# Kernel tuning notes

Hardware: AMD Instinct MI355X
Metric: run time of the kernel (lower is better)

Reference implementation:

```python
import jax, jax.numpy as jnp
import numpy as np

IN_SIZE, R = 80, 5
D = 256  # hidden size used throughout
OUT = IN_SIZE * R  # 400


def gru_cell(x, h, Wih, Whh, bih, bhh):
    # torch.nn.GRUCell semantics
    gi = x @ Wih.T + bih
    gh = h @ Whh.T + bhh
    ir, iz, in_ = jnp.split(gi, 3, axis=-1)
    hr, hz, hn = jnp.split(gh, 3, axis=-1)
    r = jax.nn.sigmoid(ir + hr)
    z = jax.nn.sigmoid(iz + hz)
    n = jnp.tanh(in_ + r * hn)
    return (1.0 - z) * n + z * h


def setup_inputs() -> dict:
    key = jax.random.key(0)
    ks = jax.random.split(key, 32)
    s = 0.05
    inp = {
        'encoder_outputs': jax.random.normal(ks[0], (128, 512, D), jnp.float32),
        'inputs': jax.random.normal(ks[1], (128, 1000, IN_SIZE), jnp.float32),
        # Prenet: Linear(400,256), Linear(256,128)
        'W1': jax.random.normal(ks[2], (256, OUT)) * s, 'b1': jnp.zeros((256,)),
        'W2': jax.random.normal(ks[3], (128, 256)) * s, 'b2': jnp.zeros((128,)),
        # attn GRUCell(384 -> 256)
        'Wih_a': jax.random.normal(ks[4], (3 * D, 128 + D)) * s,
        'Whh_a': jax.random.normal(ks[5], (3 * D, D)) * s,
        'bih_a': jnp.zeros((3 * D,)), 'bhh_a': jnp.zeros((3 * D,)),
        # Bahdanau attention: query_layer (no bias) and v: Linear(256,1,no bias)
        'Wq': jax.random.normal(ks[6], (D, D)) * s,
        'v': jax.random.normal(ks[7], (D,)) * s,
        # memory_layer Linear(256,256,no bias)
        'Wm': jax.random.normal(ks[8], (D, D)) * s,
        # pre_rnn_dec_proj Linear(512,256)
        'Wp': jax.random.normal(ks[9], (D, 2 * D)) * s, 'bp': jnp.zeros((D,)),
        # two decoder GRUCells(256 -> 256)
        'Wih_d1': jax.random.normal(ks[10], (3 * D, D)) * s,
        'Whh_d1': jax.random.normal(ks[11], (3 * D, D)) * s,
        'bih_d1': jnp.zeros((3 * D,)), 'bhh_d1': jnp.zeros((3 * D,)),
        'Wih_d2': jax.random.normal(ks[12], (3 * D, D)) * s,
        'Whh_d2': jax.random.normal(ks[13], (3 * D, D)) * s,
        'bih_d2': jnp.zeros((3 * D,)), 'bhh_d2': jnp.zeros((3 * D,)),
        # mel projection Linear(256, 400)
        'Wmel': jax.random.normal(ks[14], (OUT, D)) * s, 'bmel': jnp.zeros((OUT,)),
    }
    return inp


def reference(encoder_outputs, inputs, W1, b1, W2, b2,
              Wih_a, Whh_a, bih_a, bhh_a, Wq, v, Wm, Wp, bp,
              Wih_d1, Whh_d1, bih_d1, bhh_d1,
              Wih_d2, Whh_d2, bih_d2, bhh_d2, Wmel, bmel):
    B = encoder_outputs.shape[0]
    processed_mem = encoder_outputs @ Wm.T               # (B, T_enc, D)
    # teacher forcing: (B, T_mel, in_size) -> (T_dec, B, in_size*r)
    x = inputs.reshape(B, inputs.shape[1] // R, -1).transpose(1, 0, 2)
    # decoder input at step t is frame t-1 (zeros at t=0)
    x_shift = jnp.concatenate([jnp.zeros_like(x[:1]), x[:-1]], axis=0)

    def step(carry, x_t):
        attn_h, h1, h2, ctx = carry
        # prenet (dropout disabled: eval-mode reference)
        pre = jax.nn.relu(x_t @ W1.T + b1)
        pre = jax.nn.relu(pre @ W2.T + b2)                # (B, 128)
        cell_in = jnp.concatenate([pre, ctx], axis=-1)    # (B, 384)
        attn_h = gru_cell(cell_in, attn_h, Wih_a, Whh_a, bih_a, bhh_a)
        q = attn_h @ Wq.T                                 # (B, D)
        logits = jnp.tanh(q[:, None, :] + processed_mem) @ v  # (B, T_enc)
        align = jax.nn.softmax(logits, axis=-1)
        ctx = jnp.einsum('bt,btd->bd', align, encoder_outputs)
        dec_in = jnp.concatenate([attn_h, ctx], axis=-1) @ Wp.T + bp
        h1 = gru_cell(dec_in, h1, Wih_d1, Whh_d1, bih_d1, bhh_d1)
        dec_in = h1 + dec_in
        h2 = gru_cell(dec_in, h2, Wih_d2, Whh_d2, bih_d2, bhh_d2)
        dec_in = h2 + dec_in
        out = dec_in @ Wmel.T + bmel                      # (B, 400)
        return (attn_h, h1, h2, ctx), (out, align)

    z = jnp.zeros((B, D), encoder_outputs.dtype)
    init = (z, z, z, z)
    _, (outs, aligns) = jax.lax.scan(step, init, x_shift)
    outputs = outs.transpose(1, 0, 2)       # (B, T_dec, 400)
    alignments = aligns.transpose(1, 0, 2)  # (B, T_dec, T_enc)
    return outputs, alignments
```

## Files before the change

kernel.cpp:

```cpp
#include <hip/hip_runtime.h>

typedef _Float16 h2f __attribute__((ext_vector_type(2)));

#define LOG2E 1.44269504088896f

__device__ __forceinline__ float fexp2(float x){ return __builtin_amdgcn_exp2f(x); }
__device__ __forceinline__ float frcp (float x){ return __builtin_amdgcn_rcpf(x); }
__device__ __forceinline__ float sigm (float x){ return frcp(1.f + fexp2(-LOG2E*x)); }
__device__ __forceinline__ float tanhf2(float x){
  x = fminf(15.f, fmaxf(-15.f, x));
  float e = fexp2(2.f*LOG2E*x);
  return (e-1.f)*frcp(e+1.f);
}
__device__ __forceinline__ unsigned pkh2(float a, float b){
  h2f h; h.x = (_Float16)a; h.y = (_Float16)b;
  return __builtin_bit_cast(unsigned, h);
}

#if __has_builtin(__builtin_amdgcn_fdot2)
__device__ __forceinline__ float dot2(unsigned a, unsigned b, float c){
  return __builtin_amdgcn_fdot2(__builtin_bit_cast(h2f,a), __builtin_bit_cast(h2f,b), c, false);
}
#else
__device__ __forceinline__ float dot2(unsigned a, unsigned b, float c){
  h2f ha=__builtin_bit_cast(h2f,a), hb=__builtin_bit_cast(h2f,b);
  return c + (float)ha.x*(float)hb.x + (float)ha.y*(float)hb.y;
}
#endif

__device__ __forceinline__ void dot8_2(uint4 w, uint4 x, float& a0, float& a1){
  a0 = dot2(w.x, x.x, a0); a1 = dot2(w.y, x.y, a1);
  a0 = dot2(w.z, x.z, a0); a1 = dot2(w.w, x.w, a1);
}

template<int N, int K8>
__device__ __forceinline__ float mv(const uint4* __restrict__ W, const uint4* __restrict__ xs, int n){
  float a0 = 0.f, a1 = 0.f;
  #pragma unroll 4
  for (int k8 = 0; k8 < K8; ++k8)
    dot8_2(W[k8*N + n], xs[k8], a0, a1);
  return a0 + a1;
}

template<int N, int K8, int C>
__device__ __forceinline__ float mvc(const uint4* __restrict__ W, const uint4* __restrict__ xs, int n){
  float a0 = 0.f, a1 = 0.f;
  int k8 = 0;
  #pragma unroll 1
  for (; k8 + C <= K8; k8 += C){
    uint4 w[C];
    #pragma unroll
    for (int i = 0; i < C; ++i) w[i] = W[(size_t)(k8+i)*N + n];
    #pragma unroll
    for (int i = 0; i < C; ++i) dot8_2(w[i], xs[k8+i], a0, a1);
  }
  if constexpr (K8 % C){
    constexpr int R = K8 % C;
    uint4 w[R];
    #pragma unroll
    for (int i = 0; i < R; ++i) w[i] = W[(size_t)(k8+i)*N + n];
    #pragma unroll
    for (int i = 0; i < R; ++i) dot8_2(w[i], xs[k8+i], a0, a1);
  }
  return a0 + a1;
}

static constexpr size_t OFF_W1   = 0;
static constexpr size_t OFF_W2   = 204800;
static constexpr size_t OFF_WIHA = 270336;
static constexpr size_t OFF_WHHA = 860160;
static constexpr size_t OFF_WQ   = 1253376;
static constexpr size_t OFF_WP   = 1384448;
static constexpr size_t OFF_WD1I = 1646592;
static constexpr size_t OFF_WD1H = 2039808;
static constexpr size_t OFF_WD2I = 2433024;
static constexpr size_t OFF_WD2H = 2826240;
static constexpr size_t OFF_WMEL = 3219456;
static constexpr size_t OFF_WM   = 3424256;
static constexpr size_t OFF_TPM  = 3555328;
static constexpr size_t OFF_ENCH = 37109760;

__global__ void pack_w(const float* __restrict__ src, uint4* __restrict__ dst, int N, int K8){
  int idx = blockIdx.x*blockDim.x + threadIdx.x;
  if (idx >= N*K8) return;
  int n = idx % N, k8 = idx / N;
  const float* s = src + (size_t)n*(K8*8) + k8*8;
  dst[idx] = make_uint4(pkh2(s[0],s[1]), pkh2(s[2],s[3]), pkh2(s[4],s[5]), pkh2(s[6],s[7]));
}

__global__ void conv_enc(const float* __restrict__ enc, unsigned* __restrict__ encH){
  size_t i = blockIdx.x*(size_t)blockDim.x + threadIdx.x;
  if (i >= (size_t)128*512*128) return;
  const float2 f = *(const float2*)(enc + 2*i);
  encH[i] = pkh2(f.x, f.y);
}

__global__ __launch_bounds__(1024) void pm_kernel(const float* __restrict__ enc,
    const uint4* __restrict__ Wmp, unsigned* __restrict__ tpm)
{
  int b = blockIdx.y, tc = blockIdx.x;
  int tid = threadIdx.x;
  __shared__ __align__(16) unsigned s_e[4][128];
  if (tid < 512){
    int r = tid >> 7, d2 = tid & 127;
    const float2 f = *(const float2*)(enc + ((size_t)b*512 + tc*4 + r)*256 + 2*d2);
    s_e[r][d2] = pkh2(f.x, f.y);
  }
  __syncthreads();
  int d = tid & 255, r = tid >> 8;
  float acc = mv<256,32>(Wmp, (const uint4*)s_e[r], d);
  float tq = tanhf2(acc);
  float hi = __shfl_down(tq, 1);
  if ((d & 1) == 0)
    tpm[(size_t)b*65536 + (size_t)(d>>1)*512 + (tc*4 + r)] = pkh2(tq, hi);
}

__global__ __launch_bounds__(256) void prenet_kernel(
    const float* __restrict__ inputs,
    const float* __restrict__ b1, const float* __restrict__ b2,
    const uint4* __restrict__ W1p, const uint4* __restrict__ W2p,
    float* __restrict__ out)
{
  int t = blockIdx.x, b = blockIdx.y;
  int tid = threadIdx.x;
  __shared__ __align__(16) unsigned s_x[200];
  __shared__ __align__(16) unsigned s_p1[128];
  __shared__ float s_a[256];
  if (tid < 200){
    unsigned xv = 0u;
    if (t > 0){
      const float2 f = *(const float2*)(inputs + (size_t)b*80000 + (size_t)(t-1)*400 + 2*tid);
      xv = pkh2(f.x, f.y);
    }
    s_x[tid] = xv;
  }
  __syncthreads();
  float a = fmaxf(mv<256,50>(W1p, (const uint4*)s_x, tid) + b1[tid], 0.f);
  s_a[tid] = a;
  __syncthreads();
  if (tid < 128) s_p1[tid] = pkh2(s_a[2*tid], s_a[2*tid+1]);
  __syncthreads();
  if (tid < 128){
    float p = fmaxf(mv<128,32>(W2p, (const uint4*)s_p1, tid) + b2[tid], 0.f);
    float pN = __shfl_down(p, 1);
    if (!(tid & 1)){
      unsigned* dst = (unsigned*)(out + (size_t)10240000 + ((size_t)b*200 + t)*512);
      dst[tid>>1] = pkh2(p, pN);
    }
  }
}

__global__ __launch_bounds__(512) void mel_kernel(
    const float* __restrict__ bmel, const uint4* __restrict__ Wmelp,
    float* __restrict__ out)
{
  int t = blockIdx.x, b = blockIdx.y;
  int tid = threadIdx.x;
  __shared__ __align__(16) unsigned s_d[128];
  float* po = out + ((size_t)b*200 + t)*400;
  if (tid < 128) s_d[tid] = ((const unsigned*)po)[tid];
  __syncthreads();
  if (tid < 400){
    float r = mvc<400,32,8>(Wmelp, (const uint4*)s_d, tid) + bmel[tid];
    __builtin_nontemporal_store(r, &po[tid]);
  }
}

__global__ __launch_bounds__(1024, 1) void decoder(
   const float* __restrict__ biha, const float* __restrict__ bhha,
   const float* __restrict__ vvec, const float* __restrict__ bp,
   const float* __restrict__ bd1i, const float* __restrict__ bd1h,
   const float* __restrict__ bd2i, const float* __restrict__ bd2h,
   const uint4* __restrict__ Wihap, const uint4* __restrict__ Whhap,
   const uint4* __restrict__ Wqp, const uint4* __restrict__ Wpp,
   const uint4* __restrict__ Wd1ip, const uint4* __restrict__ Wd1hp,
   const uint4* __restrict__ Wd2ip, const uint4* __restrict__ Wd2hp,
   const unsigned* __restrict__ tpm, const unsigned* __restrict__ encH,
   float* __restrict__ out)
{
  const int tid = threadIdx.x;
  const int b = blockIdx.x;

  __shared__ __align__(16) unsigned s_cin2[192];
  __shared__ __align__(16) unsigned s_cat2[256];
  __shared__ __align__(16) unsigned s_di2[128];
  __shared__ __align__(16) unsigned s_h12[128];
  __shared__ __align__(16) unsigned s_h22[128];
  __shared__ float  s_gha[768], s_gh1[768], s_gh2[768];
  __shared__ float  s_g[768];
  __shared__ float  s_ahf[256], s_h1f[256], s_h2f[256];
  __shared__ float  s_dif[256];
  __shared__ float4 s_tv[128];
  __shared__ float  s_lp[2][512];
  __shared__ float2 s_cp[8][128];
  __shared__ float  s_mvp[4][256];
  __shared__ float  s_align[512];
  __shared__ float  s_red[16];

  if (tid < 192) s_cin2[tid] = 0u;
  if (tid < 256){ s_cat2[tid]=0u; s_ahf[tid]=0.f; s_h1f[tid]=0.f; s_h2f[tid]=0.f; }
  if (tid < 128){ s_h12[tid]=0u; s_h22[tid]=0u;
                  s_tv[tid].z = vvec[2*tid]; s_tv[tid].w = vvec[2*tid+1]; }
  __syncthreads();

  const unsigned* tpmB = tpm  + (size_t)b*65536;
  const unsigned* encB = encH + (size_t)b*65536;
  float* outMel = out + (size_t)b*200*400;
  float* outAl  = out + (size_t)10240000 + (size_t)b*200*512;

  for (int t = 0; t < 200; ++t){
    if (tid < 768){
      s_gha[tid] = mvc<768,32,8>(Whhap, (const uint4*)s_cat2, tid) + bhha[tid];
    } else if (tid < 960){
      int r = tid - 768;
      s_gh2[r] = mvc<768,32,8>(Wd2hp, (const uint4*)s_h22, r) + bd2h[r];
    } else {
      s_cin2[tid-960] = ((const unsigned*)(outAl + (size_t)t*512))[tid-960];
    }
    __syncthreads();
    if (tid < 768){
      s_gh1[tid] = mvc<768,32,8>(Wd1hp, (const uint4*)s_h12, tid) + bd1h[tid];
    } else {
      int r = 192 + tid - 768;
      s_gh2[r] = mvc<768,32,8>(Wd2hp, (const uint4*)s_h22, r) + bd2h[r];
    }
    __syncthreads();
    if (tid < 768){
      float gi = mvc<768,48,8>(Wihap, (const uint4*)s_cin2, tid) + biha[tid];
      s_g[tid] = (tid < 512) ? sigm(gi + s_gha[tid]) : gi;
    } else {
      int r = 448 + tid - 768;
      s_gh2[r] = mvc<768,32,8>(Wd2hp, (const uint4*)s_h22, r) + bd2h[r];
    }
    __syncthreads();
    if (tid < 256){
      float rr = s_g[tid], z = s_g[256+tid];
      float nv = tanhf2(s_g[512+tid] + rr*s_gha[512+tid]);
      float h  = nv + z*(s_ahf[tid] - nv);
      s_ahf[tid] = h;
      float hN = __shfl_down(h, 1);
      if (!(tid&1)) s_cat2[tid>>1] = pkh2(h, hN);
    } else if (tid < 320){
      int r = 704 + tid - 256;
      s_gh2[r] = mvc<768,32,8>(Wd2hp, (const uint4*)s_h22, r) + bd2h[r];
    }
    __syncthreads();
    if (tid < 512){
      int n = tid & 255, p = tid >> 8;
      s_mvp[p][n] = mvc<256,16,8>(Wqp + (size_t)p*16*256, (const uint4*)s_cat2 + p*16, n);
    }
    __syncthreads();
    if (tid < 256){
      float q = s_mvp[0][tid] + s_mvp[1][tid];
      ((float*)&s_tv[tid>>1])[tid&1] = tanhf2(q);
    }
    __syncthreads();
    {
      int tt = tid & 511, dh = tid >> 9;
      const unsigned* tp = tpmB + tt + (size_t)dh*32768;
      float acc = 0.f;
      #pragma unroll 1
      for (int c = 0; c < 64; c += 16){
        unsigned tw[16];
        #pragma unroll
        for (int i = 0; i < 16; ++i) tw[i] = __builtin_nontemporal_load(&tp[(size_t)(c+i)*512]);
        #pragma unroll
        for (int i = 0; i < 16; ++i){
          h2f ta = __builtin_bit_cast(h2f, tw[i]);
          float4 tv = s_tv[dh*64 + c + i];
          float ta0 = (float)ta.x, ta1 = (float)ta.y;
          acc += tv.z*(ta0+tv.x)*frcp(1.f+ta0*tv.x)
               + tv.w*(ta1+tv.y)*frcp(1.f+ta1*tv.y);
        }
      }
      s_lp[dh][tt] = acc;
    }
    __syncthreads();
    float ee = 0.f;
    if (tid < 512){
      float lg = s_lp[0][tid] + s_lp[1][tid];
      ee = fexp2(LOG2E*lg);
      float s = ee;
      #pragma unroll
      for (int off = 32; off >= 1; off >>= 1) s += __shfl_xor(s, off);
      if ((tid & 63) == 0) s_red[tid>>6] = s;
    }
    __syncthreads();
    if (tid < 512){
      float S = (s_red[0]+s_red[1])+(s_red[2]+s_red[3])
              + (s_red[4]+s_red[5])+(s_red[6]+s_red[7]);
      float a = ee * frcp(S);
      s_align[tid] = a;
      __builtin_nontemporal_store(a, &outAl[(size_t)t*512 + tid]);
    }
    __syncthreads();
    {
      int d2 = tid & 127, tc = tid >> 7;
      const unsigned* eb = encB + d2 + (size_t)tc*8192;
      float ax = 0.f, ay = 0.f;
      #pragma unroll 1
      for (int c = 0; c < 64; c += 16){
        unsigned ew[16];
        #pragma unroll
        for (int i = 0; i < 16; ++i) ew[i] = __builtin_nontemporal_load(&eb[(size_t)(c+i)*128]);
        #pragma unroll
        for (int i = 0; i < 16; ++i){
          float a = s_align[tc*64 + c + i];
          h2f e2 = __builtin_bit_cast(h2f, ew[i]);
          ax += a*(float)e2.x; ay += a*(float)e2.y;
        }
      }
      s_cp[tc][d2] = make_float2(ax, ay);
    }
    __syncthreads();
    if (tid < 256){
      const float* cp = (const float*)s_cp;
      float c = 0.f;
      #pragma unroll
      for (int k = 0; k < 8; ++k) c += cp[k*256 + tid];
      float cN = __shfl_down(c, 1);
      if (!(tid&1)){ unsigned pk = pkh2(c, cN); s_cin2[64+(tid>>1)] = pk; s_cat2[128+(tid>>1)] = pk; }
    }
    __syncthreads();
    {
      int n = tid & 255, p = tid >> 8;
      s_mvp[p][n] = mvc<256,16,8>(Wpp + (size_t)p*16*256, (const uint4*)s_cat2 + p*16, n);
    }
    __syncthreads();
    if (tid < 256){
      float di = s_mvp[0][tid]+s_mvp[1][tid]+s_mvp[2][tid]+s_mvp[3][tid] + bp[tid];
      s_dif[tid] = di;
      float dN = __shfl_down(di, 1);
      if (!(tid&1)) s_di2[tid>>1] = pkh2(di, dN);
    }
    __syncthreads();
    if (tid < 768){
      float gi = mvc<768,32,8>(Wd1ip, (const uint4*)s_di2, tid) + bd1i[tid];
      s_g[tid] = (tid < 512) ? sigm(gi + s_gh1[tid]) : gi;
    }
    __syncthreads();
    if (tid < 256){
      float rr = s_g[tid], z = s_g[256+tid];
      float nv = tanhf2(s_g[512+tid] + rr*s_gh1[512+tid]);
      float h  = nv + z*(s_h1f[tid] - nv);
      s_h1f[tid] = h;
      float di = s_dif[tid] + h; s_dif[tid] = di;
      float hN = __shfl_down(h, 1), dN = __shfl_down(di, 1);
      if (!(tid&1)){ s_h12[tid>>1] = pkh2(h, hN); s_di2[tid>>1] = pkh2(di, dN); }
    }
    __syncthreads();
    if (tid < 768){
      float gi = mvc<768,32,8>(Wd2ip, (const uint4*)s_di2, tid) + bd2i[tid];
      s_g[tid] = (tid < 512) ? sigm(gi + s_gh2[tid]) : gi;
    }
    __syncthreads();
    if (tid < 256){
      float rr = s_g[tid], z = s_g[256+tid];
      float nv = tanhf2(s_g[512+tid] + rr*s_gh2[512+tid]);
      float h  = nv + z*(s_h2f[tid] - nv);
      s_h2f[tid] = h;
      float di = s_dif[tid] + h;
      float hN = __shfl_down(h, 1), dN = __shfl_down(di, 1);
      if (!(tid&1)){
        unsigned dpk = pkh2(di, dN);
        s_h22[tid>>1] = pkh2(h, hN);
        s_di2[tid>>1] = dpk;
        ((unsigned*)(outMel + (size_t)t*400))[tid>>1] = dpk;
      }
    }
    __syncthreads();
  }
}

extern "C" void kernel_launch(void* const* d_in, const int* in_sizes, int n_in,
                              void* d_out, int out_size, void* d_ws, size_t ws_size,
                              hipStream_t stream){
  (void)in_sizes; (void)n_in; (void)out_size; (void)ws_size;
  const float* enc    = (const float*)d_in[0];
  const float* inputs = (const float*)d_in[1];
  const float* W1 = (const float*)d_in[2];   const float* b1 = (const float*)d_in[3];
  const float* W2 = (const float*)d_in[4];   const float* b2 = (const float*)d_in[5];
  const float* Wiha = (const float*)d_in[6]; const float* Whha = (const float*)d_in[7];
  const float* biha = (const float*)d_in[8]; const float* bhha = (const float*)d_in[9];
  const float* Wq = (const float*)d_in[10];  const float* v  = (const float*)d_in[11];
  const float* Wm = (const float*)d_in[12];
  const float* Wp = (const float*)d_in[13];  const float* bp = (const float*)d_in[14];
  const float* Wd1i = (const float*)d_in[15]; const float* Wd1h = (const float*)d_in[16];
  const float* bd1i = (const float*)d_in[17]; const float* bd1h = (const float*)d_in[18];
  const float* Wd2i = (const float*)d_in[19]; const float* Wd2h = (const float*)d_in[20];
  const float* bd2i = (const float*)d_in[21]; const float* bd2h = (const float*)d_in[22];
  const float* Wmel = (const float*)d_in[23]; const float* bmel = (const float*)d_in[24];

  char* ws = (char*)d_ws;
  uint4* W1p   = (uint4*)(ws + OFF_W1);
  uint4* W2p   = (uint4*)(ws + OFF_W2);
  uint4* Wihap = (uint4*)(ws + OFF_WIHA);
  uint4* Whhap = (uint4*)(ws + OFF_WHHA);
  uint4* Wqp   = (uint4*)(ws + OFF_WQ);
  uint4* Wpp   = (uint4*)(ws + OFF_WP);
  uint4* Wd1ip = (uint4*)(ws + OFF_WD1I);
  uint4* Wd1hp = (uint4*)(ws + OFF_WD1H);
  uint4* Wd2ip = (uint4*)(ws + OFF_WD2I);
  uint4* Wd2hp = (uint4*)(ws + OFF_WD2H);
  uint4* Wmelp = (uint4*)(ws + OFF_WMEL);
  uint4* Wmp   = (uint4*)(ws + OFF_WM);
  unsigned* tpm  = (unsigned*)(ws + OFF_TPM);
  unsigned* encH = (unsigned*)(ws + OFF_ENCH);

  auto P = [&](const float* s, uint4* dst, int N, int K){
    int k8 = K/8, tot = N*k8;
    pack_w<<<(tot+255)/256, 256, 0, stream>>>(s, dst, N, k8);
  };
  P(W1, W1p, 256, 400);   P(W2, W2p, 128, 256);
  P(Wiha, Wihap, 768, 384); P(Whha, Whhap, 768, 256);
  P(Wq, Wqp, 256, 256);   P(Wm, Wmp, 256, 256);
  P(Wp, Wpp, 256, 512);
  P(Wd1i, Wd1ip, 768, 256); P(Wd1h, Wd1hp, 768, 256);
  P(Wd2i, Wd2ip, 768, 256); P(Wd2h, Wd2hp, 768, 256);
  P(Wmel, Wmelp, 400, 256);

  conv_enc<<<32768, 256, 0, stream>>>(enc, encH);
  pm_kernel<<<dim3(128,128), 1024, 0, stream>>>(enc, Wmp, tpm);
  prenet_kernel<<<dim3(200,128), 256, 0, stream>>>(inputs, b1, b2, W1p, W2p, (float*)d_out);

  decoder<<<128, 1024, 0, stream>>>(
      biha, bhha, v, bp, bd1i, bd1h, bd2i, bd2h,
      Wihap, Whhap, Wqp, Wpp, Wd1ip, Wd1hp, Wd2ip, Wd2hp,
      tpm, encH, (float*)d_out);

  mel_kernel<<<dim3(200,128), 512, 0, stream>>>(bmel, Wmelp, (float*)d_out);
}
```

Measured before the change: 8.842 ms.

## Split each batch's decoder recurrence across two cooperating blocks with flag exchange

The per-batch decoder is now spread over two workgroups (256 blocks instead of 128). Each block owns half of the hidden units, half of the attention time steps and half of the context dimensions, and the two trade partial state through global memory using release/acquire flags at each step boundary. The tpm layout is reordered so attention logits can be read as uint4 vectors, and the attention score math is rewritten to use one reciprocal per pair of terms. The aim is to put twice as many CUs on the serial recurrence, since 128 blocks leave much of the GPU idle. The cost is seven spin-wait handshakes per timestep and a deadlock risk if both blocks of a pair are not resident at the same time.

```diff
diff --git a/kernel.cpp b/kernel.cpp
--- a/kernel.cpp
+++ b/kernel.cpp
@@ -45,25 +45,27 @@
 template<int N, int K8, int C>
 __device__ __forceinline__ float mvc(const uint4* __restrict__ W, const uint4* __restrict__ xs, int n){
   float a0 = 0.f, a1 = 0.f;
-  int k8 = 0;
   #pragma unroll 1
-  for (; k8 + C <= K8; k8 += C){
+  for (int k8 = 0; k8 < K8; k8 += C){
     uint4 w[C];
     #pragma unroll
     for (int i = 0; i < C; ++i) w[i] = W[(size_t)(k8+i)*N + n];
     #pragma unroll
     for (int i = 0; i < C; ++i) dot8_2(w[i], xs[k8+i], a0, a1);
   }
-  if constexpr (K8 % C){
-    constexpr int R = K8 % C;
-    uint4 w[R];
-    #pragma unroll
-    for (int i = 0; i < R; ++i) w[i] = W[(size_t)(k8+i)*N + n];
-    #pragma unroll
-    for (int i = 0; i < R; ++i) dot8_2(w[i], xs[k8+i], a0, a1);
-  }
   return a0 + a1;
 }
+
+__device__ __forceinline__ void axs(unsigned* p, unsigned v){
+  __hip_atomic_store(p, v, __ATOMIC_RELAXED, __HIP_MEMORY_SCOPE_AGENT);
+}
+__device__ __forceinline__ unsigned axl(const unsigned* p){
+  return __hip_atomic_load(p, __ATOMIC_RELAXED, __HIP_MEMORY_SCOPE_AGENT);
+}
+__device__ __forceinline__ unsigned f2u(float f){ return __builtin_bit_cast(unsigned, f); }
+__device__ __forceinline__ float u2f(unsigned u){ return __builtin_bit_cast(float, u); }
+
+__device__ __forceinline__ int grow3(int r, int HB){ return (r>>7)*256 + HB + (r & 127); }
 
 static constexpr size_t OFF_W1   = 0;
 static constexpr size_t OFF_W2   = 204800;
@@ -79,6 +81,7 @@
 static constexpr size_t OFF_WM   = 3424256;
 static constexpr size_t OFF_TPM  = 3555328;
 static constexpr size_t OFF_ENCH = 37109760;
+static constexpr size_t OFF_XCH  = 70664192;
 
 __global__ void pack_w(const float* __restrict__ src, uint4* __restrict__ dst, int N, int K8){
   int idx = blockIdx.x*blockDim.x + threadIdx.x;
@@ -111,8 +114,10 @@
   float acc = mv<256,32>(Wmp, (const uint4*)s_e[r], d);
   float tq = tanhf2(acc);
   float hi = __shfl_down(tq, 1);
-  if ((d & 1) == 0)
-    tpm[(size_t)b*65536 + (size_t)(d>>1)*512 + (tc*4 + r)] = pkh2(tq, hi);
+  if ((d & 1) == 0){
+    int t = tc*4 + r;
+    tpm[ (((size_t)b*32 + (d>>3))*512 + t)*4 + ((d>>1)&3) ] = pkh2(tq, hi);
+  }
 }
 
 __global__ __launch_bounds__(256) void prenet_kernel(
@@ -176,198 +181,303 @@
    const uint4* __restrict__ Wd1ip, const uint4* __restrict__ Wd1hp,
    const uint4* __restrict__ Wd2ip, const uint4* __restrict__ Wd2hp,
    const unsigned* __restrict__ tpm, const unsigned* __restrict__ encH,
-   float* __restrict__ out)
+   unsigned* __restrict__ xch_all, float* __restrict__ out)
 {
   const int tid = threadIdx.x;
-  const int b = blockIdx.x;
+  const int b  = blockIdx.x & 127;
+  const int H  = blockIdx.x >> 7;
+  const int HB = H*128;
+  const int PH = 1 - H;
+
+  unsigned* xch = xch_all + (size_t)b*2048;
+  unsigned* myflg = xch + H*8;
+  unsigned* paflg = xch + PH*8;
+  unsigned* xh_my   = xch + 16  + H*64;   unsigned* xh_pa   = xch + 16  + PH*64;
+  unsigned* xtq_my  = xch + 144 + H*128;  unsigned* xtq_pa  = xch + 144 + PH*128;
+  unsigned* xe_my   = xch + 400 + H*260;  unsigned* xe_pa   = xch + 400 + PH*260;
+  unsigned* xctx_my = xch + 920 + H*64;   unsigned* xctx_pa = xch + 920 + PH*64;
+  unsigned* xdi_my  = xch + 1048 + H*64;  unsigned* xdi_pa  = xch + 1048 + PH*64;
+  unsigned* xh1_my  = xch + 1176 + H*128; unsigned* xh1_pa  = xch + 1176 + PH*128;
+  unsigned* xh2_my  = xch + 1432 + H*64;  unsigned* xh2_pa  = xch + 1432 + PH*64;
 
   __shared__ __align__(16) unsigned s_cin2[192];
   __shared__ __align__(16) unsigned s_cat2[256];
   __shared__ __align__(16) unsigned s_di2[128];
   __shared__ __align__(16) unsigned s_h12[128];
   __shared__ __align__(16) unsigned s_h22[128];
-  __shared__ float  s_gha[768], s_gh1[768], s_gh2[768];
-  __shared__ float  s_g[768];
-  __shared__ float  s_ahf[256], s_h1f[256], s_h2f[256];
-  __shared__ float  s_dif[256];
+  __shared__ float  s_gha[384], s_gh1[384], s_gh2[384];
+  __shared__ float  s_p2[2][384];
+  __shared__ float  s_ahf[128], s_h1f[128], s_h2f[128];
+  __shared__ float  s_dif[128];
   __shared__ float4 s_tv[128];
-  __shared__ float  s_lp[2][512];
-  __shared__ float2 s_cp[8][128];
-  __shared__ float  s_mvp[4][256];
+  __shared__ float  s_lp[4][256];
+  __shared__ float2 s_cp[16][64];
+  __shared__ float  s_mvp[4][128];
   __shared__ float  s_align[512];
-  __shared__ float  s_red[16];
+  __shared__ float  s_red[4];
 
   if (tid < 192) s_cin2[tid] = 0u;
-  if (tid < 256){ s_cat2[tid]=0u; s_ahf[tid]=0.f; s_h1f[tid]=0.f; s_h2f[tid]=0.f; }
-  if (tid < 128){ s_h12[tid]=0u; s_h22[tid]=0u;
+  if (tid < 256) s_cat2[tid] = 0u;
+  if (tid < 128){ s_di2[tid]=0u; s_h12[tid]=0u; s_h22[tid]=0u;
+                  s_ahf[tid]=0.f; s_h1f[tid]=0.f; s_h2f[tid]=0.f;
                   s_tv[tid].z = vvec[2*tid]; s_tv[tid].w = vvec[2*tid+1]; }
   __syncthreads();
 
-  const unsigned* tpmB = tpm  + (size_t)b*65536;
   const unsigned* encB = encH + (size_t)b*65536;
-  float* outMel = out + (size_t)b*200*400;
-  float* outAl  = out + (size_t)10240000 + (size_t)b*200*512;
+  const uint4*    tpm4 = (const uint4*)tpm + (size_t)b*16384;
+  float* outMel = out + (size_t)b*80000;
+  float* outAl  = out + 10240000ull + (size_t)b*102400;
+
+  const uint4* cin4 = (const uint4*)s_cin2;
+  const uint4* cat4 = (const uint4*)s_cat2;
+  const uint4* di4  = (const uint4*)s_di2;
+  const uint4* h14  = (const uint4*)s_h12;
+  const uint4* h24  = (const uint4*)s_h22;
 
   for (int t = 0; t < 200; ++t){
-    if (tid < 768){
-      s_gha[tid] = mvc<768,32,8>(Whhap, (const uint4*)s_cat2, tid) + bhha[tid];
+    const unsigned seq = (unsigned)(t + 1);
+    if (tid < 384){
+      int g = grow3(tid, HB);
+      s_gha[tid] = mvc<768,32,8>(Whhap, cat4, g) + bhha[g];
+    } else if (tid < 768){
+      int r = tid - 384, g = grow3(r, HB);
+      s_gh1[r] = mvc<768,32,8>(Wd1hp, h14, g) + bd1h[g];
     } else if (tid < 960){
-      int r = tid - 768;
-      s_gh2[r] = mvc<768,32,8>(Wd2hp, (const uint4*)s_h22, r) + bd2h[r];
+      int r = tid - 768, g = grow3(r, HB);
+      s_gh2[r] = mvc<768,32,8>(Wd2hp, h24, g) + bd2h[g];
     } else {
       s_cin2[tid-960] = ((const unsigned*)(outAl + (size_t)t*512))[tid-960];
     }
     __syncthreads();
     if (tid < 768){
-      s_gh1[tid] = mvc<768,32,8>(Wd1hp, (const uint4*)s_h12, tid) + bd1h[tid];
-    } else {
-      int r = 192 + tid - 768;
-      s_gh2[r] = mvc<768,32,8>(Wd2hp, (const uint4*)s_h22, r) + bd2h[r];
-    }
-    __syncthreads();
-    if (tid < 768){
-      float gi = mvc<768,48,8>(Wihap, (const uint4*)s_cin2, tid) + biha[tid];
-      s_g[tid] = (tid < 512) ? sigm(gi + s_gha[tid]) : gi;
-    } else {
-      int r = 448 + tid - 768;
-      s_gh2[r] = mvc<768,32,8>(Wd2hp, (const uint4*)s_h22, r) + bd2h[r];
-    }
-    __syncthreads();
+      int p = tid/384, r = tid - p*384, g = grow3(r, HB);
+      s_p2[p][r] = mvc<768,24,8>(Wihap + (size_t)(p*24)*768, cin4 + p*24, g);
+    } else if (tid < 960){
+      int r = 192 + tid - 768, g = grow3(r, HB);
+      s_gh2[r] = mvc<768,32,8>(Wd2hp, h24, g) + bd2h[r == r ? g : g];
+    }
+    __syncthreads();
+    if (tid < 128){
+      int j = tid;
+      float gr = s_p2[0][j]     + s_p2[1][j]     + biha[HB+j]       + s_gha[j];
+      float gz = s_p2[0][128+j] + s_p2[1][128+j] + biha[256+HB+j]   + s_gha[128+j];
+      float gn = s_p2[0][256+j] + s_p2[1][256+j] + biha[512+HB+j];
+      float rr = sigm(gr), z = sigm(gz);
+      float nv = tanhf2(gn + rr*s_gha[256+j]);
+      float h  = nv + z*(s_ahf[j] - nv);
+      s_ahf[j] = h;
+      float hN = __shfl_down(h, 1);
+      if (!(j&1)){
+        unsigned pk = pkh2(h, hN);
+        s_cat2[H*64 + (j>>1)] = pk;
+        axs(xh_my + (j>>1), pk);
+      }
+    }
+    __syncthreads();
+    if (tid == 0) __hip_atomic_store(myflg+0, seq, __ATOMIC_RELEASE, __HIP_MEMORY_SCOPE_AGENT);
+    if (tid == 0){ while (__hip_atomic_load(paflg+0, __ATOMIC_ACQUIRE, __HIP_MEMORY_SCOPE_AGENT) < seq) __builtin_amdgcn_s_sleep(1); }
+    __syncthreads();
+    if (tid < 64) s_cat2[PH*64 + tid] = axl(xh_pa + tid);
+    __syncthreads();
+    if (tid < 512){
+      int r = tid & 127, p = tid >> 7;
+      s_mvp[p][r] = mvc<256,8,8>(Wqp + (size_t)(p*8)*256, cat4 + p*8, HB + r);
+    }
+    __syncthreads();
+    if (tid < 128){
+      float q = s_mvp[0][tid]+s_mvp[1][tid]+s_mvp[2][tid]+s_mvp[3][tid];
+      float tq = tanhf2(q);
+      int d = HB + tid;
+      ((float*)&s_tv[d>>1])[d&1] = tq;
+      axs(xtq_my + tid, f2u(tq));
+    }
+    __syncthreads();
+    if (tid == 0) __hip_atomic_store(myflg+1, seq, __ATOMIC_RELEASE, __HIP_MEMORY_SCOPE_AGENT);
+    if (tid == 0){ while (__hip_atomic_load(paflg+1, __ATOMIC_ACQUIRE, __HIP_MEMORY_SCOPE_AGENT) < seq) __builtin_amdgcn_s_sleep(1); }
+    __syncthreads();
+    if (tid < 128){
+      int d = PH*128 + tid;
+      ((float*)&s_tv[d>>1])[d&1] = u2f(axl(xtq_pa + tid));
+    }
+    __syncthreads();
+    {
+      int ttL = tid & 255, dh = tid >> 8;
+      const uint4* tp = tpm4 + (H*256 + ttL);
+      float acc = 0.f;
+      {
+        uint4 T[8];
+        #pragma unroll
+        for (int i = 0; i < 8; ++i) T[i] = tp[(size_t)(dh*8+i)*512];
+        #pragma unroll
+        for (int i = 0; i < 8; ++i){
+          #pragma unroll
+          for (int j = 0; j < 4; ++j){
+            unsigned u = ((const unsigned*)&T[i])[j];
+            h2f ta = __builtin_bit_cast(h2f, u);
+            float4 tv = s_tv[(dh*8+i)*4 + j];
+            float ta0 = (float)ta.x, ta1 = (float)ta.y;
+            float n0 = ta0 + tv.x, n1 = ta1 + tv.y;
+            float d0 = fmaf(ta0, tv.x, 1.f), d1 = fmaf(ta1, tv.y, 1.f);
+            float rcp = frcp(d0*d1);
+            acc = fmaf(fmaf(tv.w*n1, d0, (tv.z*n0)*d1), rcp, acc);
+          }
+        }
+      }
+      s_lp[dh][ttL] = acc;
+    }
+    __syncthreads();
+    float e_own = 0.f, S_own = 0.f;
     if (tid < 256){
-      float rr = s_g[tid], z = s_g[256+tid];
-      float nv = tanhf2(s_g[512+tid] + rr*s_gha[512+tid]);
-      float h  = nv + z*(s_ahf[tid] - nv);
-      s_ahf[tid] = h;
-      float hN = __shfl_down(h, 1);
-      if (!(tid&1)) s_cat2[tid>>1] = pkh2(h, hN);
-    } else if (tid < 320){
-      int r = 704 + tid - 256;
-      s_gh2[r] = mvc<768,32,8>(Wd2hp, (const uint4*)s_h22, r) + bd2h[r];
-    }
-    __syncthreads();
-    if (tid < 512){
-      int n = tid & 255, p = tid >> 8;
-      s_mvp[p][n] = mvc<256,16,8>(Wqp + (size_t)p*16*256, (const uint4*)s_cat2 + p*16, n);
-    }
-    __syncthreads();
-    if (tid < 256){
-      float q = s_mvp[0][tid] + s_mvp[1][tid];
-      ((float*)&s_tv[tid>>1])[tid&1] = tanhf2(q);
-    }
-    __syncthreads();
-    {
-      int tt = tid & 511, dh = tid >> 9;
-      const unsigned* tp = tpmB + tt + (size_t)dh*32768;
-      float acc = 0.f;
-      #pragma unroll 1
-      for (int c = 0; c < 64; c += 16){
-        unsigned tw[16];
-        #pragma unroll
-        for (int i = 0; i < 16; ++i) tw[i] = __builtin_nontemporal_load(&tp[(size_t)(c+i)*512]);
-        #pragma unroll
-        for (int i = 0; i < 16; ++i){
-          h2f ta = __builtin_bit_cast(h2f, tw[i]);
-          float4 tv = s_tv[dh*64 + c + i];
-          float ta0 = (float)ta.x, ta1 = (float)ta.y;
-          acc += tv.z*(ta0+tv.x)*frcp(1.f+ta0*tv.x)
-               + tv.w*(ta1+tv.y)*frcp(1.f+ta1*tv.y);
-        }
-      }
-      s_lp[dh][tt] = acc;
-    }
-    __syncthreads();
-    float ee = 0.f;
-    if (tid < 512){
-      float lg = s_lp[0][tid] + s_lp[1][tid];
-      ee = fexp2(LOG2E*lg);
-      float s = ee;
+      float lg = s_lp[0][tid]+s_lp[1][tid]+s_lp[2][tid]+s_lp[3][tid];
+      e_own = fexp2(LOG2E*lg);
+      float s = e_own;
       #pragma unroll
       for (int off = 32; off >= 1; off >>= 1) s += __shfl_xor(s, off);
       if ((tid & 63) == 0) s_red[tid>>6] = s;
     }
     __syncthreads();
-    if (tid < 512){
-      float S = (s_red[0]+s_red[1])+(s_red[2]+s_red[3])
-              + (s_red[4]+s_red[5])+(s_red[6]+s_red[7]);
-      float a = ee * frcp(S);
-      s_align[tid] = a;
-      __builtin_nontemporal_store(a, &outAl[(size_t)t*512 + tid]);
+    if (tid < 256){
+      S_own = (s_red[0]+s_red[1])+(s_red[2]+s_red[3]);
+      axs(xe_my + tid, f2u(e_own));
+      if (tid == 0) axs(xe_my + 256, f2u(S_own));
+    }
+    __syncthreads();
+    if (tid == 0) __hip_atomic_store(myflg+2, seq, __ATOMIC_RELEASE, __HIP_MEMORY_SCOPE_AGENT);
+    if (tid == 0){ while (__hip_atomic_load(paflg+2, __ATOMIC_ACQUIRE, __HIP_MEMORY_SCOPE_AGENT) < seq) __builtin_amdgcn_s_sleep(1); }
+    __syncthreads();
+    if (tid < 256){
+      float e_p = u2f(axl(xe_pa + tid));
+      float S = S_own + u2f(axl(xe_pa + 256));
+      float rS = frcp(S);
+      float a_own = e_own * rS;
+      s_align[H*256 + tid]  = a_own;
+      s_align[PH*256 + tid] = e_p * rS;
+      __builtin_nontemporal_store(a_own, &outAl[(size_t)t*512 + H*256 + tid]);
     }
     __syncthreads();
     {
-      int d2 = tid & 127, tc = tid >> 7;
-      const unsigned* eb = encB + d2 + (size_t)tc*8192;
+      int d2L = tid & 63, tc = tid >> 6;
+      int d2 = H*64 + d2L;
+      const unsigned* eb = encB + d2;
       float ax = 0.f, ay = 0.f;
       #pragma unroll 1
-      for (int c = 0; c < 64; c += 16){
-        unsigned ew[16];
+      for (int c = 0; c < 32; c += 8){
+        unsigned ew[8];
         #pragma unroll
-        for (int i = 0; i < 16; ++i) ew[i] = __builtin_nontemporal_load(&eb[(size_t)(c+i)*128]);
+        for (int i = 0; i < 8; ++i) ew[i] = eb[(size_t)(tc*32 + c + i)*128];
         #pragma unroll
-        for (int i = 0; i < 16; ++i){
-          float a = s_align[tc*64 + c + i];
+        for (int i = 0; i < 8; ++i){
+          float a = s_align[tc*32 + c + i];
           h2f e2 = __builtin_bit_cast(h2f, ew[i]);
           ax += a*(float)e2.x; ay += a*(float)e2.y;
         }
       }
-      s_cp[tc][d2] = make_float2(ax, ay);
-    }
-    __syncthreads();
-    if (tid < 256){
-      const float* cp = (const float*)s_cp;
+      s_cp[tc][d2L] = make_float2(ax, ay);
+    }
+    __syncthreads();
+    if (tid < 128){
+      int d2L = tid >> 1, comp = tid & 1;
+      const float* base = (const float*)s_cp + d2L*2 + comp;
       float c = 0.f;
       #pragma unroll
-      for (int k = 0; k < 8; ++k) c += cp[k*256 + tid];
+      for (int tc = 0; tc < 16; ++tc) c += base[(size_t)tc*128];
       float cN = __shfl_down(c, 1);
-      if (!(tid&1)){ unsigned pk = pkh2(c, cN); s_cin2[64+(tid>>1)] = pk; s_cat2[128+(tid>>1)] = pk; }
-    }
-    __syncthreads();
-    {
-      int n = tid & 255, p = tid >> 8;
-      s_mvp[p][n] = mvc<256,16,8>(Wpp + (size_t)p*16*256, (const uint4*)s_cat2 + p*16, n);
-    }
-    __syncthreads();
-    if (tid < 256){
-      float di = s_mvp[0][tid]+s_mvp[1][tid]+s_mvp[2][tid]+s_mvp[3][tid] + bp[tid];
+      if (!(tid&1)){
+        unsigned pk = pkh2(c, cN);
+        int u = H*64 + (tid>>1);
+        s_cat2[128 + u] = pk; s_cin2[64 + u] = pk;
+        axs(xctx_my + (tid>>1), pk);
+      }
+    }
+    __syncthreads();
+    if (tid == 0) __hip_atomic_store(myflg+3, seq, __ATOMIC_RELEASE, __HIP_MEMORY_SCOPE_AGENT);
+    if (tid == 0){ while (__hip_atomic_load(paflg+3, __ATOMIC_ACQUIRE, __HIP_MEMORY_SCOPE_AGENT) < seq) __builtin_amdgcn_s_sleep(1); }
+    __syncthreads();
+    if (tid < 64){
+      unsigned pk = axl(xctx_pa + tid);
+      s_cat2[128 + PH*64 + tid] = pk; s_cin2[64 + PH*64 + tid] = pk;
+    }
+    __syncthreads();
+    if (tid < 512){
+      int r = tid & 127, p = tid >> 7;
+      s_mvp[p][r] = mvc<256,16,8>(Wpp + (size_t)(p*16)*256, cat4 + p*16, HB + r);
+    }
+    __syncthreads();
+    if (tid < 128){
+      float di = s_mvp[0][tid]+s_mvp[1][tid]+s_mvp[2][tid]+s_mvp[3][tid] + bp[HB+tid];
       s_dif[tid] = di;
       float dN = __shfl_down(di, 1);
-      if (!(tid&1)) s_di2[tid>>1] = pkh2(di, dN);
-    }
+      if (!(tid&1)){
+        unsigned pk = pkh2(di, dN);
+        s_di2[H*64 + (tid>>1)] = pk;
+        axs(xdi_my + (tid>>1), pk);
+      }
+    }
+    __syncthreads();
+    if (tid == 0) __hip_atomic_store(myflg+4, seq, __ATOMIC_RELEASE, __HIP_MEMORY_SCOPE_AGENT);
+    if (tid == 0){ while (__hip_atomic_load(paflg+4, __ATOMIC_ACQUIRE, __HIP_MEMORY_SCOPE_AGENT) < seq) __builtin_amdgcn_s_sleep(1); }
+    __syncthreads();
+    if (tid < 64) s_di2[PH*64 + tid] = axl(xdi_pa + tid);
     __syncthreads();
     if (tid < 768){
-      float gi = mvc<768,32,8>(Wd1ip, (const uint4*)s_di2, tid) + bd1i[tid];
-      s_g[tid] = (tid < 512) ? sigm(gi + s_gh1[tid]) : gi;
-    }
-    __syncthreads();
-    if (tid < 256){
-      float rr = s_g[tid], z = s_g[256+tid];
-      float nv = tanhf2(s_g[512+tid] + rr*s_gh1[512+tid]);
-      float h  = nv + z*(s_h1f[tid] - nv);
-      s_h1f[tid] = h;
-      float di = s_dif[tid] + h; s_dif[tid] = di;
+      int p = tid/384, r = tid - p*384, g = grow3(r, HB);
+      s_p2[p][r] = mvc<768,16,8>(Wd1ip + (size_t)(p*16)*768, di4 + p*16, g);
+    }
+    __syncthreads();
+    if (tid < 128){
+      int j = tid;
+      float gr = s_p2[0][j]     + s_p2[1][j]     + bd1i[HB+j]     + s_gh1[j];
+      float gz = s_p2[0][128+j] + s_p2[1][128+j] + bd1i[256+HB+j] + s_gh1[128+j];
+      float gn = s_p2[0][256+j] + s_p2[1][256+j] + bd1i[512+HB+j];
+      float rr = sigm(gr), z = sigm(gz);
+      float nv = tanhf2(gn + rr*s_gh1[256+j]);
+      float h  = nv + z*(s_h1f[j] - nv);
+      s_h1f[j] = h;
+      float di = s_dif[j] + h; s_dif[j] = di;
       float hN = __shfl_down(h, 1), dN = __shfl_down(di, 1);
-      if (!(tid&1)){ s_h12[tid>>1] = pkh2(h, hN); s_di2[tid>>1] = pkh2(di, dN); }
+      if (!(j&1)){
+        unsigned hp = pkh2(h, hN), dp = pkh2(di, dN);
+        s_h12[H*64 + (j>>1)] = hp; s_di2[H*64 + (j>>1)] = dp;
+        axs(xh1_my + (j>>1), hp); axs(xh1_my + 64 + (j>>1), dp);
+      }
+    }
+    __syncthreads();
+    if (tid == 0) __hip_atomic_store(myflg+5, seq, __ATOMIC_RELEASE, __HIP_MEMORY_SCOPE_AGENT);
+    if (tid == 0){ while (__hip_atomic_load(paflg+5, __ATOMIC_ACQUIRE, __HIP_MEMORY_SCOPE_AGENT) < seq) __builtin_amdgcn_s_sleep(1); }
+    __syncthreads();
+    if (tid < 64){
+      s_h12[PH*64 + tid] = axl(xh1_pa + tid);
+      s_di2[PH*64 + tid] = axl(xh1_pa + 64 + tid);
     }
     __syncthreads();
     if (tid < 768){
-      float gi = mvc<768,32,8>(Wd2ip, (const uint4*)s_di2, tid) + bd2i[tid];
-      s_g[tid] = (tid < 512) ? sigm(gi + s_gh2[tid]) : gi;
-    }
-    __syncthreads();
-    if (tid < 256){
-      float rr = s_g[tid], z = s_g[256+tid];
-      float nv = tanhf2(s_g[512+tid] + rr*s_gh2[512+tid]);
-      float h  = nv + z*(s_h2f[tid] - nv);
-      s_h2f[tid] = h;
-      float di = s_dif[tid] + h;
+      int p = tid/384, r = tid - p*384, g = grow3(r, HB);
+      s_p2[p][r] = mvc<768,16,8>(Wd2ip + (size_t)(p*16)*768, di4 + p*16, g);
+    }
+    __syncthreads();
+    if (tid < 128){
+      int j = tid;
+      float gr = s_p2[0][j]     + s_p2[1][j]     + bd2i[HB+j]     + s_gh2[j];
+      float gz = s_p2[0][128+j] + s_p2[1][128+j] + bd2i[256+HB+j] + s_gh2[128+j];
+      float gn = s_p2[0][256+j] + s_p2[1][256+j] + bd2i[512+HB+j];
+      float rr = sigm(gr), z = sigm(gz);
+      float nv = tanhf2(gn + rr*s_gh2[256+j]);
+      float h  = nv + z*(s_h2f[j] - nv);
+      s_h2f[j] = h;
+      float di = s_dif[j] + h;
       float hN = __shfl_down(h, 1), dN = __shfl_down(di, 1);
-      if (!(tid&1)){
-        unsigned dpk = pkh2(di, dN);
-        s_h22[tid>>1] = pkh2(h, hN);
-        s_di2[tid>>1] = dpk;
-        ((unsigned*)(outMel + (size_t)t*400))[tid>>1] = dpk;
-      }
-    }
+      if (!(j&1)){
+        unsigned hp = pkh2(h, hN);
+        s_h22[H*64 + (j>>1)] = hp;
+        axs(xh2_my + (j>>1), hp);
+        ((unsigned*)(outMel + (size_t)t*400))[H*64 + (j>>1)] = pkh2(di, dN);
+      }
+    }
+    __syncthreads();
+    if (tid == 0) __hip_atomic_store(myflg+6, seq, __ATOMIC_RELEASE, __HIP_MEMORY_SCOPE_AGENT);
+    if (tid == 0){ while (__hip_atomic_load(paflg+6, __ATOMIC_ACQUIRE, __HIP_MEMORY_SCOPE_AGENT) < seq) __builtin_amdgcn_s_sleep(1); }
+    __syncthreads();
+    if (tid < 64) s_h22[PH*64 + tid] = axl(xh2_pa + tid);
     __syncthreads();
   }
 }
@@ -406,6 +516,7 @@
   uint4* Wmp   = (uint4*)(ws + OFF_WM);
   unsigned* tpm  = (unsigned*)(ws + OFF_TPM);
   unsigned* encH = (unsigned*)(ws + OFF_ENCH);
+  unsigned* xch  = (unsigned*)(ws + OFF_XCH);
 
   auto P = [&](const float* s, uint4* dst, int N, int K){
     int k8 = K/8, tot = N*k8;
@@ -419,14 +530,16 @@
   P(Wd2i, Wd2ip, 768, 256); P(Wd2h, Wd2hp, 768, 256);
   P(Wmel, Wmelp, 400, 256);
 
+  hipMemsetAsync(xch, 0, 128*2048*sizeof(unsigned), stream);
+
   conv_enc<<<32768, 256, 0, stream>>>(enc, encH);
   pm_kernel<<<dim3(128,128), 1024, 0, stream>>>(enc, Wmp, tpm);
   prenet_kernel<<<dim3(200,128), 256, 0, stream>>>(inputs, b1, b2, W1p, W2p, (float*)d_out);
 
-  decoder<<<128, 1024, 0, stream>>>(
+  decoder<<<256, 1024, 0, stream>>>(
       biha, bhha, v, bp, bd1i, bd1h, bd2i, bd2h,
       Wihap, Whhap, Wqp, Wpp, Wd1ip, Wd1hp, Wd2ip, Wd2hp,
-      tpm, encH, (float*)d_out);
+      tpm, encH, xch, (float*)d_out);
 
   mel_kernel<<<dim3(200,128), 512, 0, stream>>>(bmel, Wmelp, (float*)d_out);
 }
```

Measured after the change: 15.41 ms. 1.74x slower.

## Restructure decoder step schedule to cut barriers and fuse attention phases

Applied to the files above, without the earlier changes.

Defers the second decoder GRU's final update into the next step's first phase and redistributes the Whh_d2 matvec across idle thread slots, removing one barrier per step. The query and pre-RNN projections now split K across four threads with shuffle reductions, replacing separate shared-memory partial-sum passes. Softmax normalisation is folded into the context accumulation, which uses unnormalised exponentials, and the alignment output store moves to otherwise idle threads, removing another barrier. The processed-memory layout is changed to 16-byte vectors so each thread loads uint4, and the energy math shares one reciprocal per pair. This adds layout coupling with the pre-kernel, and the deferred GRU update makes the step logic harder to verify.

```diff
diff --git a/kernel.cpp b/kernel.cpp
--- a/kernel.cpp
+++ b/kernel.cpp
@@ -45,22 +45,13 @@
 template<int N, int K8, int C>
 __device__ __forceinline__ float mvc(const uint4* __restrict__ W, const uint4* __restrict__ xs, int n){
   float a0 = 0.f, a1 = 0.f;
-  int k8 = 0;
   #pragma unroll 1
-  for (; k8 + C <= K8; k8 += C){
+  for (int k8 = 0; k8 < K8; k8 += C){
     uint4 w[C];
     #pragma unroll
     for (int i = 0; i < C; ++i) w[i] = W[(size_t)(k8+i)*N + n];
     #pragma unroll
     for (int i = 0; i < C; ++i) dot8_2(w[i], xs[k8+i], a0, a1);
-  }
-  if constexpr (K8 % C){
-    constexpr int R = K8 % C;
-    uint4 w[R];
-    #pragma unroll
-    for (int i = 0; i < R; ++i) w[i] = W[(size_t)(k8+i)*N + n];
-    #pragma unroll
-    for (int i = 0; i < R; ++i) dot8_2(w[i], xs[k8+i], a0, a1);
   }
   return a0 + a1;
 }
@@ -111,8 +102,10 @@
   float acc = mv<256,32>(Wmp, (const uint4*)s_e[r], d);
   float tq = tanhf2(acc);
   float hi = __shfl_down(tq, 1);
-  if ((d & 1) == 0)
-    tpm[(size_t)b*65536 + (size_t)(d>>1)*512 + (tc*4 + r)] = pkh2(tq, hi);
+  if ((d & 1) == 0){
+    int t = tc*4 + r;
+    tpm[ (((size_t)b*32 + (d>>3))*512 + t)*4 + ((d>>1)&3) ] = pkh2(tq, hi);
+  }
 }
 
 __global__ __launch_bounds__(256) void prenet_kernel(
@@ -193,44 +186,58 @@
   __shared__ float4 s_tv[128];
   __shared__ float  s_lp[2][512];
   __shared__ float2 s_cp[8][128];
-  __shared__ float  s_mvp[4][256];
-  __shared__ float  s_align[512];
-  __shared__ float  s_red[16];
+  __shared__ float  s_eexp[512];
+  __shared__ float  s_red[8];
 
   if (tid < 192) s_cin2[tid] = 0u;
   if (tid < 256){ s_cat2[tid]=0u; s_ahf[tid]=0.f; s_h1f[tid]=0.f; s_h2f[tid]=0.f; }
-  if (tid < 128){ s_h12[tid]=0u; s_h22[tid]=0u;
+  if (tid < 128){ s_di2[tid]=0u; s_h12[tid]=0u; s_h22[tid]=0u;
                   s_tv[tid].z = vvec[2*tid]; s_tv[tid].w = vvec[2*tid+1]; }
   __syncthreads();
 
-  const unsigned* tpmB = tpm  + (size_t)b*65536;
   const unsigned* encB = encH + (size_t)b*65536;
-  float* outMel = out + (size_t)b*200*400;
-  float* outAl  = out + (size_t)10240000 + (size_t)b*200*512;
+  const uint4*    tpm4 = (const uint4*)tpm + (size_t)b*16384;
+  float* outMel = out + (size_t)b*80000;
+  float* outAl  = out + 10240000ull + (size_t)b*102400;
+
+  const uint4* cin4 = (const uint4*)s_cin2;
+  const uint4* cat4 = (const uint4*)s_cat2;
+  const uint4* di4  = (const uint4*)s_di2;
+  const uint4* h14  = (const uint4*)s_h12;
+  const uint4* h24  = (const uint4*)s_h22;
 
   for (int t = 0; t < 200; ++t){
     if (tid < 768){
-      s_gha[tid] = mvc<768,32,8>(Whhap, (const uint4*)s_cat2, tid) + bhha[tid];
+      s_gha[tid] = mvc<768,32,8>(Whhap, cat4, tid) + bhha[tid];
+    } else if (t > 0){
+      int i = tid - 768;
+      float rr = s_g[i], z = s_g[256+i];
+      float nv = tanhf2(s_g[512+i] + rr*s_gh2[512+i]);
+      float h  = nv + z*(s_h2f[i] - nv);
+      s_h2f[i] = h;
+      float di = s_dif[i] + h;
+      float hN = __shfl_down(h, 1), dN = __shfl_down(di, 1);
+      if (!(i&1)){
+        s_h22[i>>1] = pkh2(h, hN);
+        ((unsigned*)(outMel + (size_t)(t-1)*400))[i>>1] = pkh2(di, dN);
+      }
+    }
+    __syncthreads();
+    if (tid < 768){
+      s_gh1[tid] = mvc<768,32,8>(Wd1hp, h14, tid) + bd1h[tid];
     } else if (tid < 960){
       int r = tid - 768;
-      s_gh2[r] = mvc<768,32,8>(Wd2hp, (const uint4*)s_h22, r) + bd2h[r];
+      s_gh2[r] = mvc<768,32,8>(Wd2hp, h24, r) + bd2h[r];
     } else {
       s_cin2[tid-960] = ((const unsigned*)(outAl + (size_t)t*512))[tid-960];
     }
     __syncthreads();
     if (tid < 768){
-      s_gh1[tid] = mvc<768,32,8>(Wd1hp, (const uint4*)s_h12, tid) + bd1h[tid];
-    } else {
+      float gi = mvc<768,48,8>(Wihap, cin4, tid) + biha[tid];
+      s_g[tid] = (tid < 512) ? sigm(gi + s_gha[tid]) : gi;
+    } else if (tid < 960){
       int r = 192 + tid - 768;
-      s_gh2[r] = mvc<768,32,8>(Wd2hp, (const uint4*)s_h22, r) + bd2h[r];
-    }
-    __syncthreads();
-    if (tid < 768){
-      float gi = mvc<768,48,8>(Wihap, (const uint4*)s_cin2, tid) + biha[tid];
-      s_g[tid] = (tid < 512) ? sigm(gi + s_gha[tid]) : gi;
-    } else {
-      int r = 448 + tid - 768;
-      s_gh2[r] = mvc<768,32,8>(Wd2hp, (const uint4*)s_h22, r) + bd2h[r];
+      s_gh2[r] = mvc<768,32,8>(Wd2hp, h24, r) + bd2h[r];
     }
     __syncthreads();
     if (tid < 256){
@@ -240,61 +247,63 @@
       s_ahf[tid] = h;
       float hN = __shfl_down(h, 1);
       if (!(tid&1)) s_cat2[tid>>1] = pkh2(h, hN);
-    } else if (tid < 320){
-      int r = 704 + tid - 256;
-      s_gh2[r] = mvc<768,32,8>(Wd2hp, (const uint4*)s_h22, r) + bd2h[r];
-    }
-    __syncthreads();
-    if (tid < 512){
-      int n = tid & 255, p = tid >> 8;
-      s_mvp[p][n] = mvc<256,16,8>(Wqp + (size_t)p*16*256, (const uint4*)s_cat2 + p*16, n);
-    }
-    __syncthreads();
-    if (tid < 256){
-      float q = s_mvp[0][tid] + s_mvp[1][tid];
-      ((float*)&s_tv[tid>>1])[tid&1] = tanhf2(q);
+    } else if (tid < 448){
+      int r = 384 + tid - 256;
+      s_gh2[r] = mvc<768,32,8>(Wd2hp, h24, r) + bd2h[r];
+    }
+    __syncthreads();
+    {
+      int row = tid >> 2, kp = tid & 3;
+      float p = mvc<256,8,8>(Wqp + (size_t)(kp*8)*256, cat4 + kp*8, row);
+      p += __shfl_xor(p, 1);
+      p += __shfl_xor(p, 2);
+      if (!(tid & 3)){
+        float tq = tanhf2(p);
+        ((float*)&s_tv[row>>1])[row&1] = tq;
+      }
     }
     __syncthreads();
     {
       int tt = tid & 511, dh = tid >> 9;
-      const unsigned* tp = tpmB + tt + (size_t)dh*32768;
+      const uint4* tp = tpm4 + tt + (size_t)(dh*16)*512;
       float acc = 0.f;
       #pragma unroll 1
-      for (int c = 0; c < 64; c += 16){
-        unsigned tw[16];
+      for (int g = 0; g < 16; g += 8){
+        uint4 T[8];
         #pragma unroll
-        for (int i = 0; i < 16; ++i) tw[i] = __builtin_nontemporal_load(&tp[(size_t)(c+i)*512]);
+        for (int i = 0; i < 8; ++i) T[i] = tp[(size_t)(g+i)*512];
         #pragma unroll
-        for (int i = 0; i < 16; ++i){
-          h2f ta = __builtin_bit_cast(h2f, tw[i]);
-          float4 tv = s_tv[dh*64 + c + i];
-          float ta0 = (float)ta.x, ta1 = (float)ta.y;
-          acc += tv.z*(ta0+tv.x)*frcp(1.f+ta0*tv.x)
-               + tv.w*(ta1+tv.y)*frcp(1.f+ta1*tv.y);
+        for (int i = 0; i < 8; ++i){
+          #pragma unroll
+          for (int j = 0; j < 4; ++j){
+            unsigned u = ((const unsigned*)&T[i])[j];
+            h2f ta = __builtin_bit_cast(h2f, u);
+            float4 tv = s_tv[(dh*16 + g + i)*4 + j];
+            float ta0 = (float)ta.x, ta1 = (float)ta.y;
+            float n0 = ta0 + tv.x, n1 = ta1 + tv.y;
+            float d0 = fmaf(ta0, tv.x, 1.f), d1 = fmaf(ta1, tv.y, 1.f);
+            float r  = frcp(d0*d1);
+            acc = fmaf(fmaf(tv.w*n1, d0, (tv.z*n0)*d1), r, acc);
+          }
         }
       }
       s_lp[dh][tt] = acc;
     }
     __syncthreads();
-    float ee = 0.f;
     if (tid < 512){
       float lg = s_lp[0][tid] + s_lp[1][tid];
-      ee = fexp2(LOG2E*lg);
-      float s = ee;
+      float e = fexp2(LOG2E*lg);
+      s_eexp[tid] = e;
+      float s = e;
       #pragma unroll
       for (int off = 32; off >= 1; off >>= 1) s += __shfl_xor(s, off);
       if ((tid & 63) == 0) s_red[tid>>6] = s;
     }
     __syncthreads();
-    if (tid < 512){
-      float S = (s_red[0]+s_red[1])+(s_red[2]+s_red[3])
-              + (s_red[4]+s_red[5])+(s_red[6]+s_red[7]);
-      float a = ee * frcp(S);
-      s_align[tid] = a;
-      __builtin_nontemporal_store(a, &outAl[(size_t)t*512 + tid]);
-    }
-    __syncthreads();
     {
+      float S = ((s_red[0]+s_red[1])+(s_red[2]+s_red[3]))
+              + ((s_red[4]+s_red[5])+(s_red[6]+s_red[7]));
+      float rS = frcp(S);
       int d2 = tid & 127, tc = tid >> 7;
       const unsigned* eb = encB + d2 + (size_t)tc*8192;
       float ax = 0.f, ay = 0.f;
@@ -302,15 +311,15 @@
       for (int c = 0; c < 64; c += 16){
         unsigned ew[16];
         #pragma unroll
-        for (int i = 0; i < 16; ++i) ew[i] = __builtin_nontemporal_load(&eb[(size_t)(c+i)*128]);
+        for (int i = 0; i < 16; ++i) ew[i] = eb[(size_t)(c+i)*128];
         #pragma unroll
         for (int i = 0; i < 16; ++i){
-          float a = s_align[tc*64 + c + i];
+          float a = s_eexp[tc*64 + c + i];
           h2f e2 = __builtin_bit_cast(h2f, ew[i]);
           ax += a*(float)e2.x; ay += a*(float)e2.y;
         }
       }
-      s_cp[tc][d2] = make_float2(ax, ay);
+      s_cp[tc][d2] = make_float2(ax*rS, ay*rS);
     }
     __syncthreads();
     if (tid < 256){
@@ -320,23 +329,33 @@
       for (int k = 0; k < 8; ++k) c += cp[k*256 + tid];
       float cN = __shfl_down(c, 1);
       if (!(tid&1)){ unsigned pk = pkh2(c, cN); s_cin2[64+(tid>>1)] = pk; s_cat2[128+(tid>>1)] = pk; }
+    } else if (tid >= 512){
+      int tt = tid - 512;
+      float S = ((s_red[0]+s_red[1])+(s_red[2]+s_red[3]))
+              + ((s_red[4]+s_red[5])+(s_red[6]+s_red[7]));
+      float a = s_eexp[tt] * frcp(S);
+      __builtin_nontemporal_store(a, &outAl[(size_t)t*512 + tt]);
     }
     __syncthreads();
     {
-      int n = tid & 255, p = tid >> 8;
-      s_mvp[p][n] = mvc<256,16,8>(Wpp + (size_t)p*16*256, (const uint4*)s_cat2 + p*16, n);
-    }
-    __syncthreads();
-    if (tid < 256){
-      float di = s_mvp[0][tid]+s_mvp[1][tid]+s_mvp[2][tid]+s_mvp[3][tid] + bp[tid];
-      s_dif[tid] = di;
-      float dN = __shfl_down(di, 1);
-      if (!(tid&1)) s_di2[tid>>1] = pkh2(di, dN);
+      int row = tid >> 2, kp = tid & 3;
+      float p = mvc<256,16,8>(Wpp + (size_t)(kp*16)*256, cat4 + kp*16, row);
+      p += __shfl_xor(p, 1);
+      p += __shfl_xor(p, 2);
+      if (!(tid & 3)){
+        float di = p + bp[row];
+        s_dif[row] = di;
+        float dN = __shfl_down(di, 4);
+        if (!(tid & 7)) s_di2[row>>1] = pkh2(di, dN);
+      }
     }
     __syncthreads();
     if (tid < 768){
-      float gi = mvc<768,32,8>(Wd1ip, (const uint4*)s_di2, tid) + bd1i[tid];
+      float gi = mvc<768,32,8>(Wd1ip, di4, tid) + bd1i[tid];
       s_g[tid] = (tid < 512) ? sigm(gi + s_gh1[tid]) : gi;
+    } else if (tid < 864){
+      int r = 576 + tid - 768;
+      s_gh2[r] = mvc<768,32,8>(Wd2hp, h24, r) + bd2h[r];
     }
     __syncthreads();
     if (tid < 256){
@@ -350,25 +369,22 @@
     }
     __syncthreads();
     if (tid < 768){
-      float gi = mvc<768,32,8>(Wd2ip, (const uint4*)s_di2, tid) + bd2i[tid];
+      float gi = mvc<768,32,8>(Wd2ip, di4, tid) + bd2i[tid];
       s_g[tid] = (tid < 512) ? sigm(gi + s_gh2[tid]) : gi;
-    }
-    __syncthreads();
-    if (tid < 256){
-      float rr = s_g[tid], z = s_g[256+tid];
-      float nv = tanhf2(s_g[512+tid] + rr*s_gh2[512+tid]);
-      float h  = nv + z*(s_h2f[tid] - nv);
-      s_h2f[tid] = h;
-      float di = s_dif[tid] + h;
-      float hN = __shfl_down(h, 1), dN = __shfl_down(di, 1);
-      if (!(tid&1)){
-        unsigned dpk = pkh2(di, dN);
-        s_h22[tid>>1] = pkh2(h, hN);
-        s_di2[tid>>1] = dpk;
-        ((unsigned*)(outMel + (size_t)t*400))[tid>>1] = dpk;
-      }
-    }
-    __syncthreads();
+    } else if (tid < 864){
+      int r = 672 + tid - 768;
+      s_gh2[r] = mvc<768,32,8>(Wd2hp, h24, r) + bd2h[r];
+    }
+    __syncthreads();
+  }
+  if (tid < 256){
+    int i = tid;
+    float rr = s_g[i], z = s_g[256+i];
+    float nv = tanhf2(s_g[512+i] + rr*s_gh2[512+i]);
+    float h  = nv + z*(s_h2f[i] - nv);
+    float di = s_dif[i] + h;
+    float dN = __shfl_down(di, 1);
+    if (!(i&1)) ((unsigned*)(outMel + (size_t)199*400))[i>>1] = pkh2(di, dN);
   }
 }
 
```

Result: slower. 10.85 ms (+22.7%).
